# Optimization experiments

Hardware: AMD Instinct MI355X
Metric: run time of the kernel (lower is better)

## Reference

```python
import jax, jax.numpy as jnp
import numpy as np

B, D, C = 1024, 128, 100000
EPS = 1e-12  # torch F.normalize eps


def setup_inputs() -> dict:
    key = jax.random.key(0)
    k1, k2, k3 = jax.random.split(key, 3)
    # scale so ||x||^2 ~ 1, keeping exp(-dist) in a representable range
    xs = jax.random.normal(k1, (B, D), dtype=jnp.float32) / np.sqrt(D)
    ys = jax.random.randint(k2, (B,), 0, C, dtype=jnp.int64)
    # xavier_uniform init of Embedding(C, D): U(-a, a), a = sqrt(6/(C+D))
    a = np.sqrt(6.0 / (C + D))
    proxies = jax.random.uniform(k3, (C, D), dtype=jnp.float32, minval=-a, maxval=a)
    return {"xs": xs, "ys": ys, "proxies": proxies}


def reference(xs, ys, proxies):
    # L2-normalize every proxy (original normalizes pos proxy over dim=0 of a 1-D
    # vector and neg proxies over dim=1 -- both are per-proxy L2 normalization).
    norm = jnp.linalg.norm(proxies, axis=1, keepdims=True)
    P = proxies / jnp.maximum(norm, EPS)                      # [C, D], unit rows
    x_sq = jnp.sum(xs * xs, axis=1, keepdims=True)            # [B, 1]
    d = x_sq + 1.0 - 2.0 * (xs @ P.T)                         # [B, C]
    e = jnp.exp(-d)                                           # [B, C]
    pos = jnp.take_along_axis(e, ys[:, None], axis=1)[:, 0]   # exp(-d[b, y_b])
    neg_sum = jnp.sum(e, axis=1) - pos                        # denominator excludes the positive
    return jnp.mean(-jnp.log(pos / neg_sum))
```

## Files before the change

### kernel.cpp

```cpp
#include <hip/hip_runtime.h>
#include <hip/hip_fp16.h>

#define B_N 1024
#define D_K 128
#define C_N 100000
#define CCHUNK 80
#define NCC 1250
#define BSPLIT 2
#define NBLK_MAIN (NCC * BSPLIT)
#define NREP 8
#define EPSN 1e-12f

typedef _Float16 half8 __attribute__((ext_vector_type(8)));
typedef float floatx4 __attribute__((ext_vector_type(4)));

union U16 { uint4 u; half8 h; };

__device__ __forceinline__ unsigned int pack2h(float a, float b) {
    union { _Float16 h[2]; unsigned int u; } p;
    p.h[0] = (_Float16)a; p.h[1] = (_Float16)b;
    return p.u;
}

__global__ __launch_bounds__(256) void prep_kernel(
    const float* __restrict__ xs, const int* __restrict__ ys,
    const float* __restrict__ proxies,
    unsigned int* __restrict__ xfrag, float* __restrict__ w,
    float* __restrict__ posd, float* __restrict__ negsumR)
{
    int tid  = threadIdx.x;
    int gid  = blockIdx.x * 256 + tid;
    if (gid < B_N * NREP) negsumR[gid] = 0.0f;

    int wave = tid >> 6, lane = tid & 63;
    int b = blockIdx.x * 4 + wave;

    const float2 xv = ((const float2*)(xs + (size_t)b * D_K))[lane];
    float ss = xv.x * xv.x + xv.y * xv.y;
    #pragma unroll
    for (int m = 1; m < 64; m <<= 1) ss += __shfl_xor(ss, m, 64);
    float xsq = ss;

    {
        int f  = lane >> 4;
        int m4 = (lane >> 2) & 3;
        int j  = lane & 3;
        int idx = ((((b >> 4) * 4 + f) * 64) + ((b & 15) | (m4 << 4))) * 4 + j;
        xfrag[idx] = pack2h(2.0f * xv.x, 2.0f * xv.y);
    }

    int y = ys[b];
    const float2 pv = ((const float2*)(proxies + (size_t)y * D_K))[lane];
    float dt = xv.x * pv.x + xv.y * pv.y;
    float pp = pv.x * pv.x + pv.y * pv.y;
    #pragma unroll
    for (int m = 1; m < 64; m <<= 1) {
        dt += __shfl_xor(dt, m, 64);
        pp += __shfl_xor(pp, m, 64);
    }
    if (lane == 0) {
        w[b] = __expf(-xsq - 1.0f);
        float nrm = fmaxf(sqrtf(pp), EPSN);
        posd[b] = xsq + 1.0f - 2.0f * (dt / nrm);
    }
}

__global__ __launch_bounds__(256, 4) void main_kernel(
    const float* __restrict__ proxies,
    const uint4* __restrict__ xfrag,
    const float* __restrict__ w,
    float* __restrict__ negsumR)
{
    __shared__ uint4 ldsP[CCHUNK * 8];

    int tid = threadIdx.x;
    int bx  = blockIdx.x;
    int cc  = bx >> 1;
    int bs  = bx & 1;
    int c0  = cc * CCHUNK;

    {
        int L  = tid & 7;
        int rb = tid >> 3;
        #pragma unroll 1
        for (int pass = 0; pass < 3; ++pass) {
            int r = pass * 32 + rb;
            if (r < CCHUNK) {
                const float4* src = (const float4*)(proxies + (size_t)(c0 + r) * D_K + L * 16);
                float4 v0 = src[0], v1 = src[1], v2 = src[2], v3 = src[3];
                float ss = v0.x*v0.x + v0.y*v0.y + v0.z*v0.z + v0.w*v0.w
                         + v1.x*v1.x + v1.y*v1.y + v1.z*v1.z + v1.w*v1.w
                         + v2.x*v2.x + v2.y*v2.y + v2.z*v2.z + v2.w*v2.w
                         + v3.x*v3.x + v3.y*v3.y + v3.z*v3.z + v3.w*v3.w;
                ss += __shfl_xor(ss, 1, 64);
                ss += __shfl_xor(ss, 2, 64);
                ss += __shfl_xor(ss, 4, 64);
                float sc = 1.0f / fmaxf(sqrtf(ss), EPSN);

                union { _Float16 h[8]; uint4 u; } pa, pb;
                pa.h[0]=(_Float16)(v0.x*sc); pa.h[1]=(_Float16)(v0.y*sc);
                pa.h[2]=(_Float16)(v0.z*sc); pa.h[3]=(_Float16)(v0.w*sc);
                pa.h[4]=(_Float16)(v1.x*sc); pa.h[5]=(_Float16)(v1.y*sc);
                pa.h[6]=(_Float16)(v1.z*sc); pa.h[7]=(_Float16)(v1.w*sc);
                pb.h[0]=(_Float16)(v2.x*sc); pb.h[1]=(_Float16)(v2.y*sc);
                pb.h[2]=(_Float16)(v2.z*sc); pb.h[3]=(_Float16)(v2.w*sc);
                pb.h[4]=(_Float16)(v3.x*sc); pb.h[5]=(_Float16)(v3.y*sc);
                pb.h[6]=(_Float16)(v3.z*sc); pb.h[7]=(_Float16)(v3.w*sc);

                int cb = r >> 4, rc = r & 15;
                int f  = L >> 1;
                int mA = (L * 2) & 3;
                int mB = (L * 2 + 1) & 3;
                ldsP[(cb * 4 + f) * 64 + (rc | (mA << 4))] = pa.u;
                ldsP[(cb * 4 + f) * 64 + (rc | (mB << 4))] = pb.u;
            }
        }
    }
    __syncthreads();

    int wave  = tid >> 6, lane = tid & 63;
    int b0    = bs * 512 + wave * 128;
    int t0    = b0 >> 4;
    float* nsr = negsumR + (size_t)(bx & (NREP - 1)) * B_N;

    #pragma unroll 1
    for (int bg = 0; bg < 2; ++bg) {
        uint4 xf[4][4];
        #pragma unroll
        for (int bt = 0; bt < 4; ++bt)
            #pragma unroll
            for (int f = 0; f < 4; ++f)
                xf[bt][f] = xfrag[((t0 + bg * 4 + bt) * 4 + f) * 64 + lane];

        float s4[4] = {0.f, 0.f, 0.f, 0.f};

        #pragma unroll 1
        for (int cb = 0; cb < CCHUNK / 16; ++cb) {
            uint4 a[4];
            #pragma unroll
            for (int f = 0; f < 4; ++f)
                a[f] = ldsP[(cb * 4 + f) * 64 + lane];

            #pragma unroll
            for (int bt = 0; bt < 4; ++bt) {
                floatx4 acc = {0.f, 0.f, 0.f, 0.f};
                #pragma unroll
                for (int f = 0; f < 4; ++f) {
                    U16 ua, ub;
                    ua.u = a[f];
                    ub.u = xf[bt][f];
                    acc = __builtin_amdgcn_mfma_f32_16x16x32_f16(ua.h, ub.h, acc, 0, 0, 0);
                }
                s4[bt] += __expf(acc[0]) + __expf(acc[1])
                        + __expf(acc[2]) + __expf(acc[3]);
            }
        }

        #pragma unroll
        for (int bt = 0; bt < 4; ++bt) {
            float v = s4[bt];
            v += __shfl_xor(v, 16, 64);
            v += __shfl_xor(v, 32, 64);
            if (lane < 16) {
                int bidx = b0 + bg * 64 + bt * 16 + lane;
                atomicAdd(&nsr[bidx], v * w[bidx]);
            }
        }
    }
}

__global__ __launch_bounds__(1024) void final_kernel(
    const float* __restrict__ negsumR, const float* __restrict__ posd,
    float* __restrict__ out)
{
    __shared__ float red[1024];
    int t = threadIdx.x;
    float ns = 0.0f;
    #pragma unroll
    for (int r = 0; r < NREP; ++r) ns += negsumR[r * B_N + t];
    float pd = posd[t];
    red[t] = logf(ns - __expf(-pd)) + pd;
    __syncthreads();
    #pragma unroll
    for (int s = 512; s > 0; s >>= 1) {
        if (t < s) red[t] += red[t + s];
        __syncthreads();
    }
    if (t == 0) out[0] = red[0] * (1.0f / 1024.0f);
}

extern "C" void kernel_launch(void* const* d_in, const int* in_sizes, int n_in,
                              void* d_out, int out_size, void* d_ws, size_t ws_size,
                              hipStream_t stream)
{
    const float* xs      = (const float*)d_in[0];
    const int*   ys      = (const int*)d_in[1];
    const float* proxies = (const float*)d_in[2];

    char* ws = (char*)d_ws;
    unsigned int* xfrag = (unsigned int*)ws;
    float* w       = (float*)(ws + 262144);
    float* posd    = (float*)(ws + 262144 + 4096);
    float* negsumR = (float*)(ws + 262144 + 8192);

    prep_kernel<<<256, 256, 0, stream>>>(xs, ys, proxies, xfrag, w, posd, negsumR);
    main_kernel<<<NBLK_MAIN, 256, 0, stream>>>(proxies, (const uint4*)ws, w, negsumR);
    final_kernel<<<1, 1024, 0, stream>>>(negsumR, posd, (float*)d_out);
}
```

Baseline: 122.4 us.

## Pre-normalize proxies to fp16 fragments and switch to 32x32 MFMA tiles

Proxy normalization and fp16 packing move into the prep kernel, which writes a fragment-ordered buffer to workspace. The main kernel then streams that buffer straight into LDS with global_load_lds and computes through 32x32x16 MFMA tiles. Each block covers 160 classes by 256 batch rows, and the atomic replica count rises to 64 to cut contention. The goal is less redundant normalization, higher MFMA efficiency and fewer LDS reads per FLOP. The cost is an extra round trip through a 25.6MB fp16 proxy buffer in global memory and lower occupancy (launch bound 3).

```diff
diff --git a/kernel.cpp b/kernel.cpp
--- a/kernel.cpp
+++ b/kernel.cpp
@@ -4,15 +4,17 @@
 #define B_N 1024
 #define D_K 128
 #define C_N 100000
-#define CCHUNK 80
-#define NCC 1250
-#define BSPLIT 2
-#define NBLK_MAIN (NCC * BSPLIT)
-#define NREP 8
+#define CT_PER_CHUNK 5
+#define CCHUNK (CT_PER_CHUNK * 32)
+#define NCHUNK (C_N / CCHUNK)
+#define BSPLIT 4
+#define NBLK_MAIN (NCHUNK * BSPLIT)
+#define NREP 64
+#define NPROXY_BLK (C_N / 4)
 #define EPSN 1e-12f
 
 typedef _Float16 half8 __attribute__((ext_vector_type(8)));
-typedef float floatx4 __attribute__((ext_vector_type(4)));
+typedef float floatx16 __attribute__((ext_vector_type(16)));
 
 union U16 { uint4 u; half8 h; };
 
@@ -25,147 +27,123 @@
 __global__ __launch_bounds__(256) void prep_kernel(
     const float* __restrict__ xs, const int* __restrict__ ys,
     const float* __restrict__ proxies,
-    unsigned int* __restrict__ xfrag, float* __restrict__ w,
-    float* __restrict__ posd, float* __restrict__ negsumR)
+    unsigned int* __restrict__ pfrag, unsigned int* __restrict__ xfrag,
+    float* __restrict__ w, float* __restrict__ posd,
+    float* __restrict__ negsumR)
 {
-    int tid  = threadIdx.x;
-    int gid  = blockIdx.x * 256 + tid;
-    if (gid < B_N * NREP) negsumR[gid] = 0.0f;
+    int tid = threadIdx.x, wave = tid >> 6, lane = tid & 63;
+    int bx = blockIdx.x;
+    int ks = lane >> 3, kh = (lane >> 2) & 1, jq = lane & 3;
 
-    int wave = tid >> 6, lane = tid & 63;
-    int b = blockIdx.x * 4 + wave;
+    if (bx < NPROXY_BLK) {
+        int c = bx * 4 + wave;
+        const float2 pv = ((const float2*)(proxies + (size_t)c * D_K))[lane];
+        float ss = pv.x * pv.x + pv.y * pv.y;
+        #pragma unroll
+        for (int m = 1; m < 64; m <<= 1) ss += __shfl_xor(ss, m, 64);
+        float sc = 1.0f / fmaxf(sqrtf(ss), EPSN);
+        int idx = (((c >> 5) * 8 + ks) * 64 + ((c & 31) | (kh << 5))) * 4 + jq;
+        pfrag[idx] = pack2h(pv.x * sc, pv.y * sc);
+    } else {
+        int bb = bx - NPROXY_BLK;
+        negsumR[bb * 256 + tid] = 0.0f;
 
-    const float2 xv = ((const float2*)(xs + (size_t)b * D_K))[lane];
-    float ss = xv.x * xv.x + xv.y * xv.y;
-    #pragma unroll
-    for (int m = 1; m < 64; m <<= 1) ss += __shfl_xor(ss, m, 64);
-    float xsq = ss;
+        int b = bb * 4 + wave;
+        const float2 xv = ((const float2*)(xs + (size_t)b * D_K))[lane];
+        float ss = xv.x * xv.x + xv.y * xv.y;
+        #pragma unroll
+        for (int m = 1; m < 64; m <<= 1) ss += __shfl_xor(ss, m, 64);
+        float xsq = ss;
 
-    {
-        int f  = lane >> 4;
-        int m4 = (lane >> 2) & 3;
-        int j  = lane & 3;
-        int idx = ((((b >> 4) * 4 + f) * 64) + ((b & 15) | (m4 << 4))) * 4 + j;
+        int idx = (((b >> 5) * 8 + ks) * 64 + ((b & 31) | (kh << 5))) * 4 + jq;
         xfrag[idx] = pack2h(2.0f * xv.x, 2.0f * xv.y);
-    }
 
-    int y = ys[b];
-    const float2 pv = ((const float2*)(proxies + (size_t)y * D_K))[lane];
-    float dt = xv.x * pv.x + xv.y * pv.y;
-    float pp = pv.x * pv.x + pv.y * pv.y;
-    #pragma unroll
-    for (int m = 1; m < 64; m <<= 1) {
-        dt += __shfl_xor(dt, m, 64);
-        pp += __shfl_xor(pp, m, 64);
-    }
-    if (lane == 0) {
-        w[b] = __expf(-xsq - 1.0f);
-        float nrm = fmaxf(sqrtf(pp), EPSN);
-        posd[b] = xsq + 1.0f - 2.0f * (dt / nrm);
+        int y = ys[b];
+        const float2 pv = ((const float2*)(proxies + (size_t)y * D_K))[lane];
+        float dt = xv.x * pv.x + xv.y * pv.y;
+        float pp = pv.x * pv.x + pv.y * pv.y;
+        #pragma unroll
+        for (int m = 1; m < 64; m <<= 1) {
+            dt += __shfl_xor(dt, m, 64);
+            pp += __shfl_xor(pp, m, 64);
+        }
+        if (lane == 0) {
+            w[b] = __expf(-xsq - 1.0f);
+            float nrm = fmaxf(sqrtf(pp), EPSN);
+            posd[b] = xsq + 1.0f - 2.0f * (dt / nrm);
+        }
     }
 }
 
-__global__ __launch_bounds__(256, 4) void main_kernel(
-    const float* __restrict__ proxies,
-    const uint4* __restrict__ xfrag,
-    const float* __restrict__ w,
-    float* __restrict__ negsumR)
+__global__ __launch_bounds__(256, 3) void main_kernel(
+    const uint4* __restrict__ pfrag, const uint4* __restrict__ xfrag,
+    const float* __restrict__ w, float* __restrict__ negsumR)
 {
-    __shared__ uint4 ldsP[CCHUNK * 8];
+    __shared__ uint4 ldsP[CT_PER_CHUNK * 8 * 64];
 
-    int tid = threadIdx.x;
-    int bx  = blockIdx.x;
-    int cc  = bx >> 1;
-    int bs  = bx & 1;
-    int c0  = cc * CCHUNK;
+    int tid = threadIdx.x, wave = tid >> 6, lane = tid & 63;
+    int bx = blockIdx.x;
+    int cchunk = bx >> 2;
+    int bs = bx & 3;
 
     {
-        int L  = tid & 7;
-        int rb = tid >> 3;
-        #pragma unroll 1
-        for (int pass = 0; pass < 3; ++pass) {
-            int r = pass * 32 + rb;
-            if (r < CCHUNK) {
-                const float4* src = (const float4*)(proxies + (size_t)(c0 + r) * D_K + L * 16);
-                float4 v0 = src[0], v1 = src[1], v2 = src[2], v3 = src[3];
-                float ss = v0.x*v0.x + v0.y*v0.y + v0.z*v0.z + v0.w*v0.w
-                         + v1.x*v1.x + v1.y*v1.y + v1.z*v1.z + v1.w*v1.w
-                         + v2.x*v2.x + v2.y*v2.y + v2.z*v2.z + v2.w*v2.w
-                         + v3.x*v3.x + v3.y*v3.y + v3.z*v3.z + v3.w*v3.w;
-                ss += __shfl_xor(ss, 1, 64);
-                ss += __shfl_xor(ss, 2, 64);
-                ss += __shfl_xor(ss, 4, 64);
-                float sc = 1.0f / fmaxf(sqrtf(ss), EPSN);
-
-                union { _Float16 h[8]; uint4 u; } pa, pb;
-                pa.h[0]=(_Float16)(v0.x*sc); pa.h[1]=(_Float16)(v0.y*sc);
-                pa.h[2]=(_Float16)(v0.z*sc); pa.h[3]=(_Float16)(v0.w*sc);
-                pa.h[4]=(_Float16)(v1.x*sc); pa.h[5]=(_Float16)(v1.y*sc);
-                pa.h[6]=(_Float16)(v1.z*sc); pa.h[7]=(_Float16)(v1.w*sc);
-                pb.h[0]=(_Float16)(v2.x*sc); pb.h[1]=(_Float16)(v2.y*sc);
-                pb.h[2]=(_Float16)(v2.z*sc); pb.h[3]=(_Float16)(v2.w*sc);
-                pb.h[4]=(_Float16)(v3.x*sc); pb.h[5]=(_Float16)(v3.y*sc);
-                pb.h[6]=(_Float16)(v3.z*sc); pb.h[7]=(_Float16)(v3.w*sc);
-
-                int cb = r >> 4, rc = r & 15;
-                int f  = L >> 1;
-                int mA = (L * 2) & 3;
-                int mB = (L * 2 + 1) & 3;
-                ldsP[(cb * 4 + f) * 64 + (rc | (mA << 4))] = pa.u;
-                ldsP[(cb * 4 + f) * 64 + (rc | (mB << 4))] = pb.u;
-            }
+        const uint4* src = pfrag + (size_t)cchunk * (CT_PER_CHUNK * 8 * 64);
+        #pragma unroll
+        for (int i = 0; i < 10; ++i) {
+            int f = wave * 10 + i;
+            __builtin_amdgcn_global_load_lds(
+                (const __attribute__((address_space(1))) void*)(src + f * 64 + lane),
+                (__attribute__((address_space(3))) void*)(ldsP + f * 64),
+                16, 0, 0);
         }
     }
+
+    int nt0 = bs * 8 + wave * 2;
+    uint4 xf0[8], xf1[8];
+    #pragma unroll
+    for (int k = 0; k < 8; ++k) xf0[k] = xfrag[((nt0    ) * 8 + k) * 64 + lane];
+    #pragma unroll
+    for (int k = 0; k < 8; ++k) xf1[k] = xfrag[((nt0 + 1) * 8 + k) * 64 + lane];
+
     __syncthreads();
 
-    int wave  = tid >> 6, lane = tid & 63;
-    int b0    = bs * 512 + wave * 128;
-    int t0    = b0 >> 4;
-    float* nsr = negsumR + (size_t)(bx & (NREP - 1)) * B_N;
+    float s0 = 0.0f, s1 = 0.0f;
 
     #pragma unroll 1
-    for (int bg = 0; bg < 2; ++bg) {
-        uint4 xf[4][4];
+    for (int ct = 0; ct < CT_PER_CHUNK; ++ct) {
+        uint4 a[8];
         #pragma unroll
-        for (int bt = 0; bt < 4; ++bt)
-            #pragma unroll
-            for (int f = 0; f < 4; ++f)
-                xf[bt][f] = xfrag[((t0 + bg * 4 + bt) * 4 + f) * 64 + lane];
+        for (int k = 0; k < 8; ++k)
+            a[k] = ldsP[(ct * 8 + k) * 64 + lane];
 
-        float s4[4] = {0.f, 0.f, 0.f, 0.f};
+        floatx16 acc0, acc1;
+        #pragma unroll
+        for (int i = 0; i < 16; ++i) { acc0[i] = 0.0f; acc1[i] = 0.0f; }
 
-        #pragma unroll 1
-        for (int cb = 0; cb < CCHUNK / 16; ++cb) {
-            uint4 a[4];
-            #pragma unroll
-            for (int f = 0; f < 4; ++f)
-                a[f] = ldsP[(cb * 4 + f) * 64 + lane];
-
-            #pragma unroll
-            for (int bt = 0; bt < 4; ++bt) {
-                floatx4 acc = {0.f, 0.f, 0.f, 0.f};
-                #pragma unroll
-                for (int f = 0; f < 4; ++f) {
-                    U16 ua, ub;
-                    ua.u = a[f];
-                    ub.u = xf[bt][f];
-                    acc = __builtin_amdgcn_mfma_f32_16x16x32_f16(ua.h, ub.h, acc, 0, 0, 0);
-                }
-                s4[bt] += __expf(acc[0]) + __expf(acc[1])
-                        + __expf(acc[2]) + __expf(acc[3]);
-            }
+        #pragma unroll
+        for (int k = 0; k < 8; ++k) {
+            U16 ua, u0, u1;
+            ua.u = a[k]; u0.u = xf0[k]; u1.u = xf1[k];
+            acc0 = __builtin_amdgcn_mfma_f32_32x32x16_f16(ua.h, u0.h, acc0, 0, 0, 0);
+            acc1 = __builtin_amdgcn_mfma_f32_32x32x16_f16(ua.h, u1.h, acc1, 0, 0, 0);
         }
 
         #pragma unroll
-        for (int bt = 0; bt < 4; ++bt) {
-            float v = s4[bt];
-            v += __shfl_xor(v, 16, 64);
-            v += __shfl_xor(v, 32, 64);
-            if (lane < 16) {
-                int bidx = b0 + bg * 64 + bt * 16 + lane;
-                atomicAdd(&nsr[bidx], v * w[bidx]);
-            }
+        for (int i = 0; i < 16; ++i) {
+            s0 += __expf(acc0[i]);
+            s1 += __expf(acc1[i]);
         }
+    }
+
+    s0 += __shfl_xor(s0, 32, 64);
+    s1 += __shfl_xor(s1, 32, 64);
+
+    int rep = bx & (NREP - 1);
+    if (lane < 32) {
+        int b0 = bs * 256 + wave * 64 + lane;
+        int b1 = b0 + 32;
+        atomicAdd(&negsumR[rep * B_N + b0], s0 * w[b0]);
+        atomicAdd(&negsumR[rep * B_N + b1], s1 * w[b1]);
     }
 }
 
@@ -176,7 +154,7 @@
     __shared__ float red[1024];
     int t = threadIdx.x;
     float ns = 0.0f;
-    #pragma unroll
+    #pragma unroll 4
     for (int r = 0; r < NREP; ++r) ns += negsumR[r * B_N + t];
     float pd = posd[t];
     red[t] = logf(ns - __expf(-pd)) + pd;
@@ -198,12 +176,15 @@
     const float* proxies = (const float*)d_in[2];
 
     char* ws = (char*)d_ws;
-    unsigned int* xfrag = (unsigned int*)ws;
-    float* w       = (float*)(ws + 262144);
-    float* posd    = (float*)(ws + 262144 + 4096);
-    float* negsumR = (float*)(ws + 262144 + 8192);
+    unsigned int* pfrag   = (unsigned int*)ws;
+    unsigned int* xfrag   = (unsigned int*)(ws + 25600000);
+    float*        w       = (float*)(ws + 25600000 + 262144);
+    float*        posd    = (float*)(ws + 25600000 + 262144 + 4096);
+    float*        negsumR = (float*)(ws + 25600000 + 262144 + 8192);
 
-    prep_kernel<<<256, 256, 0, stream>>>(xs, ys, proxies, xfrag, w, posd, negsumR);
-    main_kernel<<<NBLK_MAIN, 256, 0, stream>>>(proxies, (const uint4*)ws, w, negsumR);
+    prep_kernel<<<NPROXY_BLK + 256, 256, 0, stream>>>(
+        xs, ys, proxies, pfrag, xfrag, w, posd, negsumR);
+    main_kernel<<<NBLK_MAIN, 256, 0, stream>>>(
+        (const uint4*)pfrag, (const uint4*)xfrag, w, negsumR);
     final_kernel<<<1, 1024, 0, stream>>>(negsumR, posd, (float*)d_out);
 }
```

Result: slower. 137.1 us (+12.0%).
